# Kernel optimization log

Measured on AMD Instinct MI355X. Metric: run time of the kernel, lower is better.

The kernel has to match this reference:

```python
import jax, jax.numpy as jnp
import numpy as np

B, T = 2, 512
E, NH, HD, V, P, L, KER, BLOCK = 768, 12, 64, 256, 4, 4, 16, 512
SCALE = HD ** -0.5


def _ln(x, g, b, eps=1e-5):
    m = jnp.mean(x, -1, keepdims=True)
    v = jnp.mean((x - m) ** 2, -1, keepdims=True)
    return (x - m) * jax.lax.rsqrt(v + eps) * g + b


def _rope_tables(n):
    inv = 1.0 / (10000.0 ** (jnp.arange(0, HD, 2, dtype=jnp.float32) / HD))
    f = jnp.arange(n, dtype=jnp.float32)[:, None] * inv[None, :]
    return jnp.cos(f), jnp.sin(f)


def _rope(x, cos, sin):
    # rotate over last two dims (positions, HD); split-half RoPE as in source
    h = x.shape[-1] // 2
    x1, x2 = x[..., :h], x[..., h:]
    return jnp.concatenate([x1 * cos - x2 * sin, x1 * sin + x2 * cos], axis=-1)


def _patch_attn(x, qkv_w, S):
    # x: [B,T,E]; sliding-window patch attention, step=1
    Bb, Tt, _ = x.shape
    q, k, v = jnp.split(x @ qkv_w, 3, axis=-1)
    heads = lambda t: t.reshape(Bb, Tt, NH, HD).transpose(0, 2, 1, 3)  # [B,NH,T,HD]
    q, k, v = heads(q), heads(k), heads(v)
    cos, sin = _rope_tables(Tt)
    q = _rope(q, cos, sin)
    k = _rope(k, cos, sin)
    # prefix: full causal attention over first S tokens
    sc = jnp.einsum('bnqh,bnkh->bnqk', q[:, :, :S], k[:, :, :S]) * SCALE
    mask = jnp.tril(jnp.ones((S, S), dtype=bool))
    sc = jnp.where(mask, sc, jnp.float32(-jnp.inf))
    out = jnp.einsum('bnqk,bnkh->bnqh', jax.nn.softmax(sc, axis=-1), v[:, :, :S])
    if Tt > S:
        # query t (t>=S) attends keys [t-S+1, t] (mask_sliding is all-ones for step=1)
        idx = jnp.arange(Tt - S)[:, None] + 1 + jnp.arange(S)[None, :]  # [T-S,S]
        kw = k[:, :, idx]  # [B,NH,T-S,S,HD]
        vw = v[:, :, idx]
        qs = q[:, :, S:]   # [B,NH,T-S,HD]
        sw = jnp.einsum('bnth,bntsh->bnts', qs, kw) * SCALE
        ow = jnp.einsum('bnts,bntsh->bnth', jax.nn.softmax(sw, axis=-1), vw)
        out = jnp.concatenate([out, ow], axis=2)
    return out.transpose(0, 2, 1, 3).reshape(Bb, Tt, NH * HD)


def _sa_block(x, ln0g, ln0b, ln1g, ln1b, qkv_w, proj_w, proj_b, w1, b1, w2, b2):
    # x: [B,T,P,V]; full (unmasked) attention over the P prediction slots
    Bb, Tt, Pp, _ = x.shape
    h = _ln(x, ln0g, ln0b)
    q, k, v = jnp.split(h @ qkv_w, 3, axis=-1)
    heads = lambda t: t.reshape(Bb, Tt, Pp, NH, HD).transpose(0, 1, 3, 2, 4)  # [B,T,NH,P,HD]
    q, k, v = heads(q), heads(k), heads(v)
    cos, sin = _rope_tables(Pp)
    q = _rope(q, cos, sin)
    k = _rope(k, cos, sin)
    sc = jnp.einsum('btnph,btnqh->btnpq', q, k) * SCALE
    o = jnp.einsum('btnpq,btnqh->btnph', jax.nn.softmax(sc, axis=-1), v)
    o = o.transpose(0, 1, 3, 2, 4).reshape(Bb, Tt, Pp, NH * HD)
    x = x + (o @ proj_w + proj_b)
    h2 = _ln(x, ln1g, ln1b)
    ff = jax.nn.gelu(h2 @ w1 + b1, approximate=False) @ w2 + b2
    return x + ff


def _forward(tokens, emb, blk_ln0_g, blk_ln0_b, blk_ln1_g, blk_ln1_b, blk_qkv_w,
             blk_ff_w1, blk_ff_b1, blk_ff_w2, blk_ff_b2, fin_ln_g, fin_ln_b,
             head_w, head_b, sa_ln0_g, sa_ln0_b, sa_ln1_g, sa_ln1_b, sa_qkv_w,
             sa_proj_w, sa_proj_b, sa_ff_w1, sa_ff_b1, sa_ff_w2, sa_ff_b2):
    x0 = emb[tokens]  # [B,T,E]
    x = x0
    for i in range(L):
        S = min(KER * 2 ** i, BLOCK)
        h = _ln(x, blk_ln0_g[i], blk_ln0_b[i])
        x = x + _patch_attn(h, blk_qkv_w[i], S)
        h2 = _ln(x, blk_ln1_g[i], blk_ln1_b[i])
        x = x + (jax.nn.gelu(h2 @ blk_ff_w1[i] + blk_ff_b1[i], approximate=False)
                 @ blk_ff_w2[i] + blk_ff_b2[i])
    x = x0 + x  # Golu: x = token_embedding(x); x = x + blocks(x)
    x = _ln(x, fin_ln_g, fin_ln_b)
    logits = (x @ head_w + head_b).reshape(B, T, P, V)
    logits = _sa_block(logits, sa_ln0_g, sa_ln0_b, sa_ln1_g, sa_ln1_b, sa_qkv_w,
                       sa_proj_w, sa_proj_b, sa_ff_w1, sa_ff_b1, sa_ff_w2, sa_ff_b2)
    return logits[:, :, 0, :]  # [B,T,V] (y is None path)


def setup_inputs() -> dict:
    key = jax.random.key(0)
    ks = jax.random.split(key, 12)
    w = lambda k, sh: jax.random.normal(k, sh, dtype=jnp.float32) * 0.02
    return {
        'tokens': jax.random.randint(ks[0], (B, T), 0, V),
        'emb': w(ks[1], (V, E)),
        'blk_ln0_g': jnp.ones((L, E), jnp.float32),
        'blk_ln0_b': jnp.zeros((L, E), jnp.float32),
        'blk_ln1_g': jnp.ones((L, E), jnp.float32),
        'blk_ln1_b': jnp.zeros((L, E), jnp.float32),
        'blk_qkv_w': w(ks[2], (L, E, 3 * E)),
        'blk_ff_w1': w(ks[3], (L, E, 4 * E)),
        'blk_ff_b1': jnp.zeros((L, 4 * E), jnp.float32),
        'blk_ff_w2': w(ks[4], (L, 4 * E, E)),
        'blk_ff_b2': jnp.zeros((L, E), jnp.float32),
        'fin_ln_g': jnp.ones((E,), jnp.float32),
        'fin_ln_b': jnp.zeros((E,), jnp.float32),
        'head_w': w(ks[5], (E, V * P)),
        'head_b': jnp.zeros((V * P,), jnp.float32),
        'sa_ln0_g': jnp.ones((V,), jnp.float32),
        'sa_ln0_b': jnp.zeros((V,), jnp.float32),
        'sa_ln1_g': jnp.ones((V,), jnp.float32),
        'sa_ln1_b': jnp.zeros((V,), jnp.float32),
        'sa_qkv_w': w(ks[6], (V, 3 * E)),
        'sa_proj_w': w(ks[7], (E, V)),
        'sa_proj_b': jnp.zeros((V,), jnp.float32),
        'sa_ff_w1': w(ks[8], (V, 4 * V)),
        'sa_ff_b1': jnp.zeros((4 * V,), jnp.float32),
        'sa_ff_w2': w(ks[9], (4 * V, V)),
        'sa_ff_b2': jnp.zeros((V,), jnp.float32),
    }


def reference(tokens, emb, blk_ln0_g, blk_ln0_b, blk_ln1_g, blk_ln1_b, blk_qkv_w,
              blk_ff_w1, blk_ff_b1, blk_ff_w2, blk_ff_b2, fin_ln_g, fin_ln_b,
              head_w, head_b, sa_ln0_g, sa_ln0_b, sa_ln1_g, sa_ln1_b, sa_qkv_w,
              sa_proj_w, sa_proj_b, sa_ff_w1, sa_ff_b1, sa_ff_w2, sa_ff_b2):
    return _forward(tokens, emb, blk_ln0_g, blk_ln0_b, blk_ln1_g, blk_ln1_b,
                    blk_qkv_w, blk_ff_w1, blk_ff_b1, blk_ff_w2, blk_ff_b2,
                    fin_ln_g, fin_ln_b, head_w, head_b, sa_ln0_g, sa_ln0_b,
                    sa_ln1_g, sa_ln1_b, sa_qkv_w, sa_proj_w, sa_proj_b,
                    sa_ff_w1, sa_ff_b1, sa_ff_w2, sa_ff_b2)
```

## Files before the change

### kernel.cpp

```cpp
#include <hip/hip_runtime.h>
#include <hip/hip_bf16.h>
#include <cstdint>
#include <cstddef>

#define BB    2
#define TSEQ  512
#define EDIM  768
#define NHEAD 12
#define HDIM  64
#define VDIM  256
#define PDIM  4
#define NROW  (BB*TSEQ)
#define NROW2 (BB*TSEQ*PDIM)

typedef __attribute__((ext_vector_type(8))) short short8;
typedef __attribute__((ext_vector_type(4))) short short4v;
typedef __attribute__((ext_vector_type(4))) float floatx4;

__device__ __forceinline__ float gelu_f(float v){
    return 0.5f * v * (1.0f + erff(v * 0.70710678118654752f));
}
__device__ __forceinline__ float b2f(short s){
    unsigned u = ((unsigned)(unsigned short)s) << 16;
    float f; __builtin_memcpy(&f, &u, 4); return f;
}
__device__ __forceinline__ short f2bs(float v){
    __hip_bfloat16 h = __float2bfloat16(v);
    short s; __builtin_memcpy(&s, &h, 2); return s;
}
__device__ __forceinline__ void gload16(const void* g, void* l){
    __builtin_amdgcn_global_load_lds((const __attribute__((address_space(1))) void*)g,
                                     (__attribute__((address_space(3))) void*)l, 16, 0, 0);
}

#define WAITN(n) asm volatile("s_waitcnt vmcnt(" #n ")" ::: "memory")
#define WAIT_STAGE(rem, full, half)                         \
    do{ if((rem) >= 2)      WAITN(full);                    \
        else if((rem) == 1) WAITN(half);                    \
        else                WAITN(0);                       \
        asm volatile("s_barrier" ::: "memory"); }while(0)

struct WD2 { const float* in; __hip_bfloat16* out; int K; int N; int nt; };
struct WDs { WD2 d[17]; };

__global__ __launch_bounds__(256) void wconv_all(WDs a)
{
    int id = blockIdx.x;
    int i = 0;
    while(i < 16 && id >= a.d[i].nt){ id -= a.d[i].nt; i++; }
    WD2 w = a.d[i];
    const int tx = w.N / 128;
    const int n0 = (id % tx) * 128, k0 = (id / tx) * 128;
    __shared__ short t[128*128];
    {
        const int c4 = (threadIdx.x & 31) * 4;
        const int r0 = threadIdx.x >> 5;
        #pragma unroll
        for(int half = 0; half < 2; half++){
            float4 v[8];
            #pragma unroll
            for(int it = 0; it < 8; it++){
                int r = r0 + it*8 + half*64;
                v[it] = *(const float4*)(w.in + (size_t)(k0 + r) * w.N + n0 + c4);
            }
            #pragma unroll
            for(int it = 0; it < 8; it++){
                int r = r0 + it*8 + half*64;
                int nswz = c4 ^ (((r >> 3) & 15) << 2);
                short4v o;
                o[0] = f2bs(v[it].x); o[1] = f2bs(v[it].y);
                o[2] = f2bs(v[it].z); o[3] = f2bs(v[it].w);
                *(short4v*)&t[r*128 + nswz] = o;
            }
        }
    }
    __syncthreads();
    {
        const int k8 = (threadIdx.x & 15) * 8;
        const int nr = threadIdx.x >> 4;
        const int swz = (k8 >> 3) << 2;
        #pragma unroll
        for(int pass = 0; pass < 8; pass++){
            int n = nr + pass*16;
            int nswz = n ^ swz;
            short8 o;
            #pragma unroll
            for(int j = 0; j < 8; j++) o[j] = t[(k8 + j)*128 + nswz];
            *(short8*)((short*)w.out + (size_t)(n0 + n) * w.K + k0 + k8) = o;
        }
    }
}

template<int ACT, int RESID, int OUTBF16, int ROPESA>
__global__ __launch_bounds__(256) void gemm128(
    const short* __restrict__ A, const short* __restrict__ Bt,
    const float* __restrict__ bias, const float* __restrict__ resid,
    void* __restrict__ Cout, const float* __restrict__ rc, const float* __restrict__ rs,
    int M, int N, int K)
{
    alignas(16) __shared__ short As[4*128*32];
    alignas(16) __shared__ short Bs[4*128*32];
    const int tid  = threadIdx.x;
    const int lane = tid & 63;
    const int wave = tid >> 6;
    const int bm = blockIdx.y * 128, bn = blockIdx.x * 128;
    const int wm = (wave >> 1) * 64, wn = (wave & 1) * 64;
    const int quad = lane >> 4, l16 = lane & 15;

    floatx4 acc[4][4];
    #pragma unroll
    for(int i = 0; i < 4; i++)
        #pragma unroll
        for(int j = 0; j < 4; j++)
            acc[i][j] = floatx4{0.f, 0.f, 0.f, 0.f};

    const int r  = tid >> 2;
    const int c8 = (tid & 3) * 8;
    const int ldsoff = (tid & 192) * 16;

    auto issue = [&](int k0, int cur){
        char* ab = (char*)As + cur*8192 + ldsoff;
        char* bb = (char*)Bs + cur*8192 + ldsoff;
        gload16(A  + (size_t)(bm + r     ) * K + k0 + c8, ab);
        gload16(A  + (size_t)(bm + r + 64) * K + k0 + c8, ab + 4096);
        gload16(Bt + (size_t)(bn + r     ) * K + k0 + c8, bb);
        gload16(Bt + (size_t)(bn + r + 64) * K + k0 + c8, bb + 4096);
    };

    const int niter = K >> 5;
    issue(0, 0); issue(32, 1); issue(64, 2);
    for(int it = 0; it < niter; it++){
        WAIT_STAGE(niter - 1 - it, 8, 4);
        if(it + 3 < niter) issue((it + 3) << 5, (it + 3) & 3);
        const short* Ab = As + (it & 3) * 4096;
        const short* Bb = Bs + (it & 3) * 4096;
        short8 af[4], bfr[4];
        #pragma unroll
        for(int i = 0; i < 4; i++){
            af[i]  = *(const short8*)&Ab[(wm + i*16 + l16)*32 + quad*8];
            bfr[i] = *(const short8*)&Bb[(wn + i*16 + l16)*32 + quad*8];
        }
        #pragma unroll
        for(int i = 0; i < 4; i++)
            #pragma unroll
            for(int j = 0; j < 4; j++)
                acc[i][j] = __builtin_amdgcn_mfma_f32_16x16x32_bf16(af[i], bfr[j], acc[i][j], 0, 0, 0);
    }

    float* Cf = (float*)Cout;
    __hip_bfloat16* Cb = (__hip_bfloat16*)Cout;

    if(ROPESA){
        const int hb = bn + wn;
        const int region = hb / 768;
        #pragma unroll
        for(int i = 0; i < 4; i++){
            #pragma unroll
            for(int rr = 0; rr < 4; rr++){
                int row = bm + wm + i*16 + quad*4 + rr;
                float a0 = acc[i][0][rr], a1 = acc[i][1][rr];
                float a2 = acc[i][2][rr], a3 = acc[i][3][rr];
                size_t rowb = (size_t)row * N + hb;
                if(region == 2){
                    Cb[rowb + l16]      = __float2bfloat16(a0);
                    Cb[rowb + 16 + l16] = __float2bfloat16(a1);
                    Cb[rowb + 32 + l16] = __float2bfloat16(a2);
                    Cb[rowb + 48 + l16] = __float2bfloat16(a3);
                }else{
                    int p = row & 3;
                    float c0 = rc[p*32 + l16],      s0 = rs[p*32 + l16];
                    float c1 = rc[p*32 + 16 + l16], s1 = rs[p*32 + 16 + l16];
                    Cb[rowb + l16]      = __float2bfloat16(a0*c0 - a2*s0);
                    Cb[rowb + 16 + l16] = __float2bfloat16(a1*c1 - a3*s1);
                    Cb[rowb + 32 + l16] = __float2bfloat16(a0*s0 + a2*c0);
                    Cb[rowb + 48 + l16] = __float2bfloat16(a1*s1 + a3*c1);
                }
            }
        }
        return;
    }

    #pragma unroll
    for(int i = 0; i < 4; i++){
        int row0 = bm + wm + i*16 + quad*4;
        #pragma unroll
        for(int j = 0; j < 4; j++){
            int col = bn + wn + j*16 + l16;
            float bv = bias ? bias[col] : 0.f;
            #pragma unroll
            for(int rr = 0; rr < 4; rr++){
                float v = acc[i][j][rr] + bv;
                if(ACT) v = gelu_f(v);
                if(RESID) v += resid[(size_t)(row0 + rr) * N + col];
                if(OUTBF16) Cb[(size_t)(row0 + rr) * N + col] = __float2bfloat16(v);
                else        Cf[(size_t)(row0 + rr) * N + col] = v;
            }
        }
    }
}

template<int EPI>
__global__ __launch_bounds__(256) void gemm64x128(
    const short* __restrict__ A, const short* __restrict__ Bt,
    const float* __restrict__ bias, __hip_bfloat16* __restrict__ Cout,
    __hip_bfloat16* __restrict__ qrb, __hip_bfloat16* __restrict__ krb,
    __hip_bfloat16* __restrict__ vvb,
    const float* __restrict__ rc, const float* __restrict__ rs,
    int M, int N, int K)
{
    alignas(16) __shared__ short As[4*64*32];
    alignas(16) __shared__ short Bs[4*128*32];
    const int tid  = threadIdx.x;
    const int lane = tid & 63;
    const int wave = tid >> 6;
    const int bm = blockIdx.y * 64, bn = blockIdx.x * 128;
    const int wm = (wave >> 1) * 32, wn = (wave & 1) * 64;
    const int quad = lane >> 4, l16 = lane & 15;

    floatx4 acc[2][4];
    #pragma unroll
    for(int i = 0; i < 2; i++)
        #pragma unroll
        for(int j = 0; j < 4; j++)
            acc[i][j] = floatx4{0.f, 0.f, 0.f, 0.f};

    const int r  = tid >> 2;
    const int c8 = (tid & 3) * 8;
    const int ldsoff = (tid & 192) * 16;

    auto issue = [&](int k0, int cur){
        char* ab = (char*)As + cur*4096 + ldsoff;
        char* bb = (char*)Bs + cur*8192 + ldsoff;
        gload16(A  + (size_t)(bm + r     ) * K + k0 + c8, ab);
        gload16(Bt + (size_t)(bn + r     ) * K + k0 + c8, bb);
        gload16(Bt + (size_t)(bn + r + 64) * K + k0 + c8, bb + 4096);
    };

    const int niter = K >> 5;
    issue(0, 0); issue(32, 1); issue(64, 2);
    for(int it = 0; it < niter; it++){
        WAIT_STAGE(niter - 1 - it, 6, 3);
        if(it + 3 < niter) issue((it + 3) << 5, (it + 3) & 3);
        const short* Ab = As + (it & 3) * 2048;
        const short* Bb = Bs + (it & 3) * 4096;
        short8 af[2], bfr[4];
        #pragma unroll
        for(int i = 0; i < 2; i++)
            af[i]  = *(const short8*)&Ab[(wm + i*16 + l16)*32 + quad*8];
        #pragma unroll
        for(int j = 0; j < 4; j++)
            bfr[j] = *(const short8*)&Bb[(wn + j*16 + l16)*32 + quad*8];
        #pragma unroll
        for(int i = 0; i < 2; i++)
            #pragma unroll
            for(int j = 0; j < 4; j++)
                acc[i][j] = __builtin_amdgcn_mfma_f32_16x16x32_bf16(af[i], bfr[j], acc[i][j], 0, 0, 0);
    }

    if(EPI == 2){
        const int hb = bn + wn;
        const int region = hb / 768;
        const int h = (hb % 768) >> 6;
        #pragma unroll
        for(int i = 0; i < 2; i++){
            #pragma unroll
            for(int rr = 0; rr < 4; rr++){
                int row = bm + wm + i*16 + quad*4 + rr;
                int t = row & (TSEQ-1), b = row >> 9;
                float a0 = acc[i][0][rr], a1 = acc[i][1][rr];
                float a2 = acc[i][2][rr], a3 = acc[i][3][rr];
                size_t dbase = ((size_t)(b*NHEAD + h)*TSEQ + t)*HDIM;
                if(region == 2){
                    vvb[dbase + l16]      = __float2bfloat16(a0);
                    vvb[dbase + 16 + l16] = __float2bfloat16(a1);
                    vvb[dbase + 32 + l16] = __float2bfloat16(a2);
                    vvb[dbase + 48 + l16] = __float2bfloat16(a3);
                }else{
                    float c0 = rc[t*32 + l16],      s0 = rs[t*32 + l16];
                    float c1 = rc[t*32 + 16 + l16], s1 = rs[t*32 + 16 + l16];
                    __hip_bfloat16* dst = (region == 0) ? qrb : krb;
                    dst[dbase + l16]      = __float2bfloat16(a0*c0 - a2*s0);
                    dst[dbase + 16 + l16] = __float2bfloat16(a1*c1 - a3*s1);
                    dst[dbase + 32 + l16] = __float2bfloat16(a0*s0 + a2*c0);
                    dst[dbase + 48 + l16] = __float2bfloat16(a1*s1 + a3*c1);
                }
            }
        }
        return;
    }

    #pragma unroll
    for(int i = 0; i < 2; i++){
        int row0 = bm + wm + i*16 + quad*4;
        #pragma unroll
        for(int j = 0; j < 4; j++){
            int col = bn + wn + j*16 + l16;
            float bv = bias ? bias[col] : 0.f;
            #pragma unroll
            for(int rr = 0; rr < 4; rr++){
                float v = acc[i][j][rr] + bv;
                if(EPI == 1) v = gelu_f(v);
                Cout[(size_t)(row0 + rr) * N + col] = __float2bfloat16(v);
            }
        }
    }
}

template<int RESID, int OUTC>
__global__ __launch_bounds__(256) void gemm64t(
    const short* __restrict__ A, const short* __restrict__ Bt,
    const float* __restrict__ bias, const float* __restrict__ resid,
    float* __restrict__ Cf, float* __restrict__ outp, int M, int N, int K)
{
    alignas(16) __shared__ short As[4*64*32];
    alignas(16) __shared__ short Bs[4*64*32];
    const int tid  = threadIdx.x;
    const int lane = tid & 63;
    const int wave = tid >> 6;
    const int bm = blockIdx.y * 64, bn = blockIdx.x * 64;
    const int wm = (wave >> 1) * 32, wn = (wave & 1) * 32;
    const int quad = lane >> 4, l16 = lane & 15;

    floatx4 acc[2][2];
    #pragma unroll
    for(int i = 0; i < 2; i++)
        #pragma unroll
        for(int j = 0; j < 2; j++)
            acc[i][j] = floatx4{0.f, 0.f, 0.f, 0.f};

    const int r  = tid >> 2;
    const int c8 = (tid & 3) * 8;
    const int ldsoff = (tid & 192) * 16;

    auto issue = [&](int k0, int cur){
        char* ab = (char*)As + cur*4096 + ldsoff;
        char* bb = (char*)Bs + cur*4096 + ldsoff;
        gload16(A  + (size_t)(bm + r) * K + k0 + c8, ab);
        gload16(Bt + (size_t)(bn + r) * K + k0 + c8, bb);
    };

    const int niter = K >> 5;
    issue(0, 0); issue(32, 1); issue(64, 2);
    for(int it = 0; it < niter; it++){
        WAIT_STAGE(niter - 1 - it, 4, 2);
        if(it + 3 < niter) issue((it + 3) << 5, (it + 3) & 3);
        const short* Ab = As + (it & 3) * 2048;
        const short* Bb = Bs + (it & 3) * 2048;
        short8 af[2], bfr[2];
        #pragma unroll
        for(int i = 0; i < 2; i++){
            af[i]  = *(const short8*)&Ab[(wm + i*16 + l16)*32 + quad*8];
            bfr[i] = *(const short8*)&Bb[(wn + i*16 + l16)*32 + quad*8];
        }
        #pragma unroll
        for(int i = 0; i < 2; i++)
            #pragma unroll
            for(int j = 0; j < 2; j++)
                acc[i][j] = __builtin_amdgcn_mfma_f32_16x16x32_bf16(af[i], bfr[j], acc[i][j], 0, 0, 0);
    }

    #pragma unroll
    for(int i = 0; i < 2; i++){
        int row0 = bm + wm + i*16 + quad*4;
        #pragma unroll
        for(int j = 0; j < 2; j++){
            int col = bn + wn + j*16 + l16;
            float bv = bias ? bias[col] : 0.f;
            #pragma unroll
            for(int rr = 0; rr < 4; rr++){
                int row = row0 + rr;
                float v = acc[i][j][rr] + bv;
                if(RESID) v += resid[(size_t)row * N + col];
                Cf[(size_t)row * N + col] = v;
                if(OUTC && (row & 3) == 0)
                    outp[(size_t)(row >> 2) * N + col] = v;
            }
        }
    }
}

template<int D>
__global__ __launch_bounds__(256) void ln_wave(
    const float* __restrict__ in, const float* __restrict__ in2,
    const float* __restrict__ g, const float* __restrict__ bta,
    __hip_bfloat16* __restrict__ out)
{
    constexpr int NC = D / 256;
    const int row  = blockIdx.x * 4 + (threadIdx.x >> 6);
    const int lane = threadIdx.x & 63;
    const float* xr = in + (size_t)row * D;
    float4 v[NC];
    float sum = 0.f, sq = 0.f;
    #pragma unroll
    for(int j = 0; j < NC; j++){
        int d0 = (lane + 64*j) * 4;
        v[j] = *(const float4*)(xr + d0);
        if(in2){
            float4 u = *(const float4*)(in2 + (size_t)row * D + d0);
            v[j].x += u.x; v[j].y += u.y; v[j].z += u.z; v[j].w += u.w;
        }
        sum += v[j].x + v[j].y + v[j].z + v[j].w;
        sq  += v[j].x*v[j].x + v[j].y*v[j].y + v[j].z*v[j].z + v[j].w*v[j].w;
    }
    #pragma unroll
    for(int off = 32; off > 0; off >>= 1){
        sum += __shfl_xor(sum, off, 64);
        sq  += __shfl_xor(sq,  off, 64);
    }
    const float m    = sum / D;
    const float rstd = rsqrtf(fmaxf(sq / D - m*m, 0.f) + 1e-5f);
    #pragma unroll
    for(int j = 0; j < NC; j++){
        int d0 = (lane + 64*j) * 4;
        float4 gg = *(const float4*)(g + d0);
        float4 bb = *(const float4*)(bta + d0);
        short4v o;
        o[0] = f2bs((v[j].x - m) * rstd * gg.x + bb.x);
        o[1] = f2bs((v[j].y - m) * rstd * gg.y + bb.y);
        o[2] = f2bs((v[j].z - m) * rstd * gg.z + bb.z);
        o[3] = f2bs((v[j].w - m) * rstd * gg.w + bb.w);
        *(short4v*)((short*)out + (size_t)row * D + d0) = o;
    }
}

__global__ __launch_bounds__(192) void embed_kernel(
    const int* __restrict__ tokens, const float* __restrict__ emb,
    float* __restrict__ x0, float* __restrict__ x)
{
    const int row = blockIdx.x;
    const int tok = tokens[row];
    const float4* src = (const float4*)(emb + (size_t)tok * EDIM);
    float4* d0 = (float4*)(x0 + (size_t)row * EDIM);
    float4* d1 = (float4*)(x  + (size_t)row * EDIM);
    for(int i = threadIdx.x; i < EDIM/4; i += blockDim.x){
        float4 v = src[i]; d0[i] = v; d1[i] = v;
    }
}

__global__ __launch_bounds__(256) void rope_kernel(float* __restrict__ rc, float* __restrict__ rs)
{
    int i = blockIdx.x * 256 + threadIdx.x;
    int pos = i >> 5, d = i & 31;
    float inv = powf(10000.0f, -(float)(2*d) / 64.0f);
    float f = (float)pos * inv;
    rc[i] = cosf(f);
    rs[i] = sinf(f);
}

template<int S>
__global__ __launch_bounds__(256) void patch_attn2(
    const __hip_bfloat16* __restrict__ qr, const __hip_bfloat16* __restrict__ kr,
    const __hip_bfloat16* __restrict__ vv, float* __restrict__ x)
{
    constexpr int W = S + 3;
    alignas(16) __shared__ short Ks[W*64];
    alignas(16) __shared__ short Vs[W*64];
    __shared__ float qlds[4*64];
    __shared__ float pb[4*128];

    const int t0 = blockIdx.x * 4;
    const int h = blockIdx.y, b = blockIdx.z;
    const int tid = threadIdx.x;
    const int wv = tid >> 6, lane = tid & 63;
    const size_t headbase = ((size_t)(b*NHEAD + h)) * TSEQ;

    const int c = tid & 7;
    for(int r = tid >> 3; r < W; r += 32){
        int g = t0 - S + 1 + r;
        int gc = g < 0 ? 0 : g;
        int sc = (c ^ (r & 7)) * 8;
        *(short8*)&Ks[r*64 + sc] = *(const short8*)((const short*)kr + (headbase + gc)*64 + c*8);
        *(short8*)&Vs[r*64 + sc] = *(const short8*)((const short*)vv + (headbase + gc)*64 + c*8);
    }
    qlds[wv*64 + lane] = __bfloat162float(qr[(headbase + t0 + wv)*64 + lane]);
    __syncthreads();

    const int t = t0 + wv;
    const int r0 = (S >= 64) ? (wv + lane) : ((lane < S) ? (wv + lane) : 0);
    const int r1 = wv + lane + 64;
    float a0 = 0.f, a1 = 0.f;
    #pragma unroll
    for(int ch = 0; ch < 8; ch++){
        float4 qa = *(const float4*)&qlds[wv*64 + ch*8];
        float4 qb = *(const float4*)&qlds[wv*64 + ch*8 + 4];
        short8 k0 = *(const short8*)&Ks[r0*64 + ((ch ^ (r0 & 7))*8)];
        a0 += qa.x*b2f(k0[0]) + qa.y*b2f(k0[1]) + qa.z*b2f(k0[2]) + qa.w*b2f(k0[3])
            + qb.x*b2f(k0[4]) + qb.y*b2f(k0[5]) + qb.z*b2f(k0[6]) + qb.w*b2f(k0[7]);
        if(S == 128){
            short8 k1 = *(const short8*)&Ks[r1*64 + ((ch ^ (r1 & 7))*8)];
            a1 += qa.x*b2f(k1[0]) + qa.y*b2f(k1[1]) + qa.z*b2f(k1[2]) + qa.w*b2f(k1[3])
                + qb.x*b2f(k1[4]) + qb.y*b2f(k1[5]) + qb.z*b2f(k1[6]) + qb.w*b2f(k1[7]);
        }
    }
    const int key0 = t - S + 1 + lane;
    const bool v0 = (lane < S) && (key0 >= 0);
    const bool v1 = (S == 128) && (key0 + 64 >= 0);
    float s0 = v0 ? a0 * 0.125f : -1e30f;
    float s1 = v1 ? a1 * 0.125f : -1e30f;
    float mx = fmaxf(s0, s1);
    #pragma unroll
    for(int off = 32; off > 0; off >>= 1) mx = fmaxf(mx, __shfl_xor(mx, off, 64));
    float p0 = v0 ? expf(s0 - mx) : 0.f;
    float p1 = v1 ? expf(s1 - mx) : 0.f;
    float sm = p0 + p1;
    #pragma unroll
    for(int off = 32; off > 0; off >>= 1) sm += __shfl_xor(sm, off, 64);
    const float inv = 1.f / sm;
    pb[wv*128 + lane] = p0 * inv;
    if(S == 128) pb[wv*128 + lane + 64] = p1 * inv;
    __syncthreads();

    const int d = lane;
    const int coff = d >> 3, dlo = d & 7;
    float o = 0.f;
    #pragma unroll 8
    for(int j = 0; j < S; j++){
        int r = wv + j;
        float p = pb[wv*128 + j];
        o += p * b2f(Vs[r*64 + ((coff ^ (r & 7))*8) + dlo]);
    }
    x[((size_t)(b*TSEQ) + t) * EDIM + h*HDIM + d] += o;
}

__global__ __launch_bounds__(256) void sa_attn(
    const __hip_bfloat16* __restrict__ qkv2, __hip_bfloat16* __restrict__ o)
{
    const int t = blockIdx.x, h = blockIdx.y, b = blockIdx.z;
    const int p = threadIdx.x >> 6, lane = threadIdx.x & 63;
    const int row0 = (b*TSEQ + t) * PDIM;
    const short* base = (const short*)qkv2 + (size_t)row0 * (3*EDIM);
    const int d = lane;
    float q = b2f(base[(size_t)p*(3*EDIM) + h*HDIM + d]);
    float sc[4];
    #pragma unroll
    for(int j = 0; j < 4; j++){
        float kj = b2f(base[(size_t)j*(3*EDIM) + EDIM + h*HDIM + d]);
        float v = q * kj;
        #pragma unroll
        for(int off = 32; off > 0; off >>= 1) v += __shfl_xor(v, off, 64);
        sc[j] = v * 0.125f;
    }
    float m = fmaxf(fmaxf(sc[0], sc[1]), fmaxf(sc[2], sc[3]));
    float e0 = expf(sc[0]-m), e1 = expf(sc[1]-m), e2 = expf(sc[2]-m), e3 = expf(sc[3]-m);
    float idn = 1.f / (e0 + e1 + e2 + e3);
    float ov = (e0 * b2f(base[0*(3*EDIM) + 2*EDIM + h*HDIM + d])
              + e1 * b2f(base[1*(3*EDIM) + 2*EDIM + h*HDIM + d])
              + e2 * b2f(base[2*(3*EDIM) + 2*EDIM + h*HDIM + d])
              + e3 * b2f(base[3*(3*EDIM) + 2*EDIM + h*HDIM + d])) * idn;
    o[(size_t)(row0 + p) * EDIM + h*HDIM + d] = __float2bfloat16(ov);
}

extern "C" void kernel_launch(void* const* d_in, const int* in_sizes, int n_in,
                              void* d_out, int out_size, void* d_ws, size_t ws_size,
                              hipStream_t stream)
{
    const int*   tokens    = (const int*)  d_in[0];
    const float* emb       = (const float*)d_in[1];
    const float* bl0g      = (const float*)d_in[2];
    const float* bl0b      = (const float*)d_in[3];
    const float* bl1g      = (const float*)d_in[4];
    const float* bl1b      = (const float*)d_in[5];
    const float* qkv_w     = (const float*)d_in[6];
    const float* ff_w1     = (const float*)d_in[7];
    const float* ff_b1     = (const float*)d_in[8];
    const float* ff_w2     = (const float*)d_in[9];
    const float* ff_b2     = (const float*)d_in[10];
    const float* fin_g     = (const float*)d_in[11];
    const float* fin_b     = (const float*)d_in[12];
    const float* head_w    = (const float*)d_in[13];
    const float* head_b    = (const float*)d_in[14];
    const float* sa_ln0_g  = (const float*)d_in[15];
    const float* sa_ln0_b  = (const float*)d_in[16];
    const float* sa_ln1_g  = (const float*)d_in[17];
    const float* sa_ln1_b  = (const float*)d_in[18];
    const float* sa_qkv_w  = (const float*)d_in[19];
    const float* sa_proj_w = (const float*)d_in[20];
    const float* sa_proj_b = (const float*)d_in[21];
    const float* sa_ff_w1  = (const float*)d_in[22];
    const float* sa_ff_b1  = (const float*)d_in[23];
    const float* sa_ff_w2  = (const float*)d_in[24];
    const float* sa_ff_b2  = (const float*)d_in[25];
    float* out = (float*)d_out;

    char* p = (char*)d_ws;
    auto alloc = [&](size_t bytes){ char* q = p; p += (bytes + 255) & ~(size_t)255; return q; };

    float* logits = (float*)alloc((size_t)NROW2*VDIM*4);
    float* ropec  = (float*)alloc(512*32*4);
    float* ropes  = (float*)alloc(512*32*4);
    __hip_bfloat16* wqkvT[4]; for(int i=0;i<4;i++) wqkvT[i] = (__hip_bfloat16*)alloc((size_t)768*2304*2);
    __hip_bfloat16* wff1T[4]; for(int i=0;i<4;i++) wff1T[i] = (__hip_bfloat16*)alloc((size_t)768*3072*2);
    __hip_bfloat16* wff2T[4]; for(int i=0;i<4;i++) wff2T[i] = (__hip_bfloat16*)alloc((size_t)3072*768*2);
    __hip_bfloat16* wheadT   = (__hip_bfloat16*)alloc((size_t)768*1024*2);
    __hip_bfloat16* wsaqkvT  = (__hip_bfloat16*)alloc((size_t)256*2304*2);
    __hip_bfloat16* wsaprojT = (__hip_bfloat16*)alloc((size_t)768*256*2);
    __hip_bfloat16* wsaff1T  = (__hip_bfloat16*)alloc((size_t)256*1024*2);
    __hip_bfloat16* wsaff2T  = (__hip_bfloat16*)alloc((size_t)1024*256*2);
    char* U = p;
    float* x0           = (float*)(U);
    float* x            = (float*)(U + 3145728);
    __hip_bfloat16* h   = (__hip_bfloat16*)(U + 6291456);
    __hip_bfloat16* ff1 = (__hip_bfloat16*)(U + 7864320);
    __hip_bfloat16* qrb = (__hip_bfloat16*)(U + 14155776);
    __hip_bfloat16* krb = (__hip_bfloat16*)(U + 15728640);
    __hip_bfloat16* vvb = (__hip_bfloat16*)(U + 17301504);
    __hip_bfloat16* h2    = (__hip_bfloat16*)(U);
    __hip_bfloat16* qkv2  = (__hip_bfloat16*)(U + 2097152);
    __hip_bfloat16* sa_o  = (__hip_bfloat16*)(U + 20971520);
    __hip_bfloat16* sa_f1 = (__hip_bfloat16*)(U + 27262976);

    embed_kernel<<<NROW, 192, 0, stream>>>(tokens, emb, x0, x);
    rope_kernel<<<64, 256, 0, stream>>>(ropec, ropes);
    {
        WDs wds; int tot = 0, n = 0;
        auto add = [&](const float* in, __hip_bfloat16* o2, int K, int N){
            wds.d[n++] = WD2{in, o2, K, N, (N/128)*(K/128)};
            tot += (N/128)*(K/128);
        };
        for(int i=0;i<4;i++){
            add(qkv_w + (size_t)i*768*2304, wqkvT[i], 768, 2304);
            add(ff_w1 + (size_t)i*768*3072, wff1T[i], 768, 3072);
            add(ff_w2 + (size_t)i*3072*768, wff2T[i], 3072, 768);
        }
        add(head_w,    wheadT,   768, 1024);
        add(sa_qkv_w,  wsaqkvT,  256, 2304);
        add(sa_proj_w, wsaprojT, 768, 256);
        add(sa_ff_w1,  wsaff1T,  256, 1024);
        add(sa_ff_w2,  wsaff2T, 1024, 256);
        wconv_all<<<tot, 256, 0, stream>>>(wds);
    }

    for(int i = 0; i < 4; i++){
        ln_wave<EDIM><<<NROW/4, 256, 0, stream>>>(x, nullptr, bl0g + i*EDIM, bl0b + i*EDIM, h);
        gemm64x128<2><<<dim3(18, 16), 256, 0, stream>>>(
            (const short*)h, (const short*)wqkvT[i], nullptr, nullptr,
            qrb, krb, vvb, ropec, ropes, NROW, 3*EDIM, EDIM);
        dim3 agrid(TSEQ/4, NHEAD, BB);
        if(i == 0)      patch_attn2<16><<<agrid, 256, 0, stream>>>(qrb, krb, vvb, x);
        else if(i == 1) patch_attn2<32><<<agrid, 256, 0, stream>>>(qrb, krb, vvb, x);
        else if(i == 2) patch_attn2<64><<<agrid, 256, 0, stream>>>(qrb, krb, vvb, x);
        else            patch_attn2<128><<<agrid, 256, 0, stream>>>(qrb, krb, vvb, x);
        ln_wave<EDIM><<<NROW/4, 256, 0, stream>>>(x, nullptr, bl1g + i*EDIM, bl1b + i*EDIM, h);
        gemm64x128<1><<<dim3(24, 16), 256, 0, stream>>>(
            (const short*)h, (const short*)wff1T[i], ff_b1 + (size_t)i*4*EDIM, ff1,
            nullptr, nullptr, nullptr, nullptr, nullptr, NROW, 4*EDIM, EDIM);
        gemm64t<1,0><<<dim3(12, 16), 256, 0, stream>>>(
            (const short*)ff1, (const short*)wff2T[i], ff_b2 + (size_t)i*EDIM, x, x, nullptr,
            NROW, EDIM, 4*EDIM);
    }

    ln_wave<EDIM><<<NROW/4, 256, 0, stream>>>(x, x0, fin_g, fin_b, h);
    gemm64t<0,0><<<dim3(16, 16), 256, 0, stream>>>(
        (const short*)h, (const short*)wheadT, head_b, nullptr, logits, nullptr,
        NROW, PDIM*VDIM, EDIM);

    ln_wave<VDIM><<<NROW2/4, 256, 0, stream>>>(logits, nullptr, sa_ln0_g, sa_ln0_b, h2);
    gemm128<0,0,1,1><<<dim3(18, 32), 256, 0, stream>>>(
        (const short*)h2, (const short*)wsaqkvT, nullptr, nullptr, qkv2,
        ropec, ropes, NROW2, 3*EDIM, VDIM);
    sa_attn<<<dim3(TSEQ, NHEAD, BB), 256, 0, stream>>>(qkv2, sa_o);
    gemm64t<1,0><<<dim3(4, 64), 256, 0, stream>>>(
        (const short*)sa_o, (const short*)wsaprojT, sa_proj_b, logits, logits, nullptr,
        NROW2, VDIM, EDIM);
    ln_wave<VDIM><<<NROW2/4, 256, 0, stream>>>(logits, nullptr, sa_ln1_g, sa_ln1_b, h2);
    gemm128<1,0,1,0><<<dim3(8, 32), 256, 0, stream>>>(
        (const short*)h2, (const short*)wsaff1T, sa_ff_b1, nullptr, sa_f1,
        nullptr, nullptr, NROW2, 4*VDIM, VDIM);
    gemm64t<1,1><<<dim3(4, 64), 256, 0, stream>>>(
        (const short*)sa_f1, (const short*)wsaff2T, sa_ff_b2, logits, logits, out,
        NROW2, VDIM, 4*VDIM);
}
```

Measured before the change: 691.6 us.

## Process sixteen queries per patch-attention block to reuse the K/V window

The sliding-window patch attention kernel now handles 16 consecutive query positions per block instead of 4, with each wave looping over 4 queries. The shared K/V window grows from S+3 to S+15 rows, so each staged key/value row serves more queries and redundant global K/V loads fall. Because each wave now reads only the probability rows it wrote itself, the block barrier between softmax and the PV product is dropped. The trade-off is a grid four times smaller and more serial work per wave, which can reduce latency hiding.

```diff
diff --git a/kernel.cpp b/kernel.cpp
--- a/kernel.cpp
+++ b/kernel.cpp
@@ -448,17 +448,17 @@
 }
 
 template<int S>
-__global__ __launch_bounds__(256) void patch_attn2(
+__global__ __launch_bounds__(256) void patch_attn16(
     const __hip_bfloat16* __restrict__ qr, const __hip_bfloat16* __restrict__ kr,
     const __hip_bfloat16* __restrict__ vv, float* __restrict__ x)
 {
-    constexpr int W = S + 3;
+    constexpr int W = S + 15;
     alignas(16) __shared__ short Ks[W*64];
     alignas(16) __shared__ short Vs[W*64];
-    __shared__ float qlds[4*64];
-    __shared__ float pb[4*128];
-
-    const int t0 = blockIdx.x * 4;
+    __shared__ float qlds[16*64];
+    __shared__ float pb[16*128];
+
+    const int t0 = blockIdx.x * 16;
     const int h = blockIdx.y, b = blockIdx.z;
     const int tid = threadIdx.x;
     const int wv = tid >> 6, lane = tid & 63;
@@ -472,54 +472,62 @@
         *(short8*)&Ks[r*64 + sc] = *(const short8*)((const short*)kr + (headbase + gc)*64 + c*8);
         *(short8*)&Vs[r*64 + sc] = *(const short8*)((const short*)vv + (headbase + gc)*64 + c*8);
     }
-    qlds[wv*64 + lane] = __bfloat162float(qr[(headbase + t0 + wv)*64 + lane]);
+    for(int i = tid; i < 16*64; i += 256)
+        qlds[i] = __bfloat162float(qr[(headbase + t0 + (i >> 6))*64 + (i & 63)]);
     __syncthreads();
 
-    const int t = t0 + wv;
-    const int r0 = (S >= 64) ? (wv + lane) : ((lane < S) ? (wv + lane) : 0);
-    const int r1 = wv + lane + 64;
-    float a0 = 0.f, a1 = 0.f;
-    #pragma unroll
-    for(int ch = 0; ch < 8; ch++){
-        float4 qa = *(const float4*)&qlds[wv*64 + ch*8];
-        float4 qb = *(const float4*)&qlds[wv*64 + ch*8 + 4];
-        short8 k0 = *(const short8*)&Ks[r0*64 + ((ch ^ (r0 & 7))*8)];
-        a0 += qa.x*b2f(k0[0]) + qa.y*b2f(k0[1]) + qa.z*b2f(k0[2]) + qa.w*b2f(k0[3])
-            + qb.x*b2f(k0[4]) + qb.y*b2f(k0[5]) + qb.z*b2f(k0[6]) + qb.w*b2f(k0[7]);
-        if(S == 128){
-            short8 k1 = *(const short8*)&Ks[r1*64 + ((ch ^ (r1 & 7))*8)];
-            a1 += qa.x*b2f(k1[0]) + qa.y*b2f(k1[1]) + qa.z*b2f(k1[2]) + qa.w*b2f(k1[3])
-                + qb.x*b2f(k1[4]) + qb.y*b2f(k1[5]) + qb.z*b2f(k1[6]) + qb.w*b2f(k1[7]);
-        }
-    }
-    const int key0 = t - S + 1 + lane;
-    const bool v0 = (lane < S) && (key0 >= 0);
-    const bool v1 = (S == 128) && (key0 + 64 >= 0);
-    float s0 = v0 ? a0 * 0.125f : -1e30f;
-    float s1 = v1 ? a1 * 0.125f : -1e30f;
-    float mx = fmaxf(s0, s1);
-    #pragma unroll
-    for(int off = 32; off > 0; off >>= 1) mx = fmaxf(mx, __shfl_xor(mx, off, 64));
-    float p0 = v0 ? expf(s0 - mx) : 0.f;
-    float p1 = v1 ? expf(s1 - mx) : 0.f;
-    float sm = p0 + p1;
-    #pragma unroll
-    for(int off = 32; off > 0; off >>= 1) sm += __shfl_xor(sm, off, 64);
-    const float inv = 1.f / sm;
-    pb[wv*128 + lane] = p0 * inv;
-    if(S == 128) pb[wv*128 + lane + 64] = p1 * inv;
-    __syncthreads();
+    #pragma unroll
+    for(int qq = 0; qq < 4; qq++){
+        const int ql = wv*4 + qq;
+        const int t  = t0 + ql;
+        const int r0 = (S >= 64) ? (ql + lane) : ((lane < S) ? (ql + lane) : 0);
+        const int r1 = ql + lane + 64;
+        float a0 = 0.f, a1 = 0.f;
+        #pragma unroll
+        for(int ch = 0; ch < 8; ch++){
+            float4 qa = *(const float4*)&qlds[ql*64 + ch*8];
+            float4 qb = *(const float4*)&qlds[ql*64 + ch*8 + 4];
+            short8 k0 = *(const short8*)&Ks[r0*64 + ((ch ^ (r0 & 7))*8)];
+            a0 += qa.x*b2f(k0[0]) + qa.y*b2f(k0[1]) + qa.z*b2f(k0[2]) + qa.w*b2f(k0[3])
+                + qb.x*b2f(k0[4]) + qb.y*b2f(k0[5]) + qb.z*b2f(k0[6]) + qb.w*b2f(k0[7]);
+            if(S == 128){
+                short8 k1 = *(const short8*)&Ks[r1*64 + ((ch ^ (r1 & 7))*8)];
+                a1 += qa.x*b2f(k1[0]) + qa.y*b2f(k1[1]) + qa.z*b2f(k1[2]) + qa.w*b2f(k1[3])
+                    + qb.x*b2f(k1[4]) + qb.y*b2f(k1[5]) + qb.z*b2f(k1[6]) + qb.w*b2f(k1[7]);
+            }
+        }
+        const int key0 = t - S + 1 + lane;
+        const bool v0 = (lane < S) && (key0 >= 0);
+        const bool v1 = (S == 128) && (key0 + 64 >= 0);
+        float s0 = v0 ? a0 * 0.125f : -1e30f;
+        float s1 = v1 ? a1 * 0.125f : -1e30f;
+        float mx = fmaxf(s0, s1);
+        #pragma unroll
+        for(int off = 32; off > 0; off >>= 1) mx = fmaxf(mx, __shfl_xor(mx, off, 64));
+        float p0 = v0 ? expf(s0 - mx) : 0.f;
+        float p1 = v1 ? expf(s1 - mx) : 0.f;
+        float sm = p0 + p1;
+        #pragma unroll
+        for(int off = 32; off > 0; off >>= 1) sm += __shfl_xor(sm, off, 64);
+        const float inv = 1.f / sm;
+        pb[ql*128 + lane] = p0 * inv;
+        if(S == 128) pb[ql*128 + lane + 64] = p1 * inv;
+    }
 
     const int d = lane;
     const int coff = d >> 3, dlo = d & 7;
-    float o = 0.f;
-    #pragma unroll 8
-    for(int j = 0; j < S; j++){
-        int r = wv + j;
-        float p = pb[wv*128 + j];
-        o += p * b2f(Vs[r*64 + ((coff ^ (r & 7))*8) + dlo]);
-    }
-    x[((size_t)(b*TSEQ) + t) * EDIM + h*HDIM + d] += o;
+    #pragma unroll
+    for(int qq = 0; qq < 4; qq++){
+        const int ql = wv*4 + qq;
+        float o = 0.f;
+        #pragma unroll 8
+        for(int j = 0; j < S; j++){
+            int r = ql + j;
+            float p = pb[ql*128 + j];
+            o += p * b2f(Vs[r*64 + ((coff ^ (r & 7))*8) + dlo]);
+        }
+        x[((size_t)(b*TSEQ) + t0 + ql) * EDIM + h*HDIM + d] += o;
+    }
 }
 
 __global__ __launch_bounds__(256) void sa_attn(
@@ -635,11 +643,11 @@
         gemm64x128<2><<<dim3(18, 16), 256, 0, stream>>>(
             (const short*)h, (const short*)wqkvT[i], nullptr, nullptr,
             qrb, krb, vvb, ropec, ropes, NROW, 3*EDIM, EDIM);
-        dim3 agrid(TSEQ/4, NHEAD, BB);
-        if(i == 0)      patch_attn2<16><<<agrid, 256, 0, stream>>>(qrb, krb, vvb, x);
-        else if(i == 1) patch_attn2<32><<<agrid, 256, 0, stream>>>(qrb, krb, vvb, x);
-        else if(i == 2) patch_attn2<64><<<agrid, 256, 0, stream>>>(qrb, krb, vvb, x);
-        else            patch_attn2<128><<<agrid, 256, 0, stream>>>(qrb, krb, vvb, x);
+        dim3 agrid(TSEQ/16, NHEAD, BB);
+        if(i == 0)      patch_attn16<16><<<agrid, 256, 0, stream>>>(qrb, krb, vvb, x);
+        else if(i == 1) patch_attn16<32><<<agrid, 256, 0, stream>>>(qrb, krb, vvb, x);
+        else if(i == 2) patch_attn16<64><<<agrid, 256, 0, stream>>>(qrb, krb, vvb, x);
+        else            patch_attn16<128><<<agrid, 256, 0, stream>>>(qrb, krb, vvb, x);
         ln_wave<EDIM><<<NROW/4, 256, 0, stream>>>(x, nullptr, bl1g + i*EDIM, bl1b + i*EDIM, h);
         gemm64x128<1><<<dim3(24, 16), 256, 0, stream>>>(
             (const short*)h, (const short*)wff1T[i], ff_b1 + (size_t)i*4*EDIM, ff1,
```

New measurement: 698.8 us. Within noise of the previous version (+1.1%).
